# Optimization experiments

Hardware: AMD Instinct MI355X
Metric: run time of the kernel (lower is better)

Reference implementation:

```python
import jax, jax.numpy as jnp
import numpy as np

B, S, E, H = 2, 2048, 2048, 16
HD = E // H  # head dim (value_factor = 1, so key dim == value dim)
EPS = 1e-5


def setup_inputs() -> dict:
    key = jax.random.key(0)
    ks = jax.random.split(key, 12)
    std = 0.02

    def lin(k, din, dout):
        kw, kb = jax.random.split(k)
        W = jax.random.normal(kw, (din, dout), jnp.float32) * std  # stored [in,out]
        b = jnp.zeros((dout,), jnp.float32)
        return W, b

    x = jax.random.normal(ks[0], (B, S, E), jnp.float32)
    Wq, bq = lin(ks[1], E, E)
    Wk, bk = lin(ks[2], E, E)
    Wv, bv = lin(ks[3], E, E)
    Wg, bg = lin(ks[4], E, E)
    Wo, bo = lin(ks[5], E, E)
    gn_w = jnp.ones((E,), jnp.float32)
    gn_b = jnp.zeros((E,), jnp.float32)
    decay = jnp.log(1.0 - 2.0 ** (-5.0 - jnp.arange(H, dtype=jnp.float32)))
    return dict(x=x, Wq=Wq, bq=bq, Wk=Wk, bk=bk, Wv=Wv, bv=bv,
                Wg=Wg, bg=bg, Wo=Wo, bo=bo, gn_w=gn_w, gn_b=gn_b, decay=decay)


def _retention(x, Wq, bq, Wk, bk, Wv, bv, Wg, bg, Wo, bo, gn_w, gn_b, decay):
    b, s, e = x.shape
    h = decay.shape[0]
    hd = e // h
    scaling = hd ** -0.5

    def heads(t):  # [b, s, e] -> [b, h, s, hd]
        return t.reshape(b, s, h, hd).transpose(0, 2, 1, 3)

    q = heads((x @ Wq + bq) * scaling)
    k = heads(x @ Wk + bk)
    v = heads(x @ Wv + bv)

    # causal decay mask D[h,i,j] = gamma_h^(i-j) for i>=j, else 0
    idx = jnp.arange(s)
    diff = idx[:, None] - idx[None, :]               # [s, s]
    causal = diff >= 0
    diff_c = jnp.where(causal, diff, 0).astype(jnp.float32)
    D = jnp.where(causal[None], jnp.exp(decay[:, None, None] * diff_c[None]), 0.0)  # [h,s,s]

    ret = jnp.einsum('bhid,bhjd->bhij', q, k) * D[None]      # [b,h,s,s]
    # per-row abs-sum normalization (detached scale, clamped at 1)
    scale = jnp.clip(jnp.abs(jax.lax.stop_gradient(ret).sum(-1, keepdims=True)), 1.0, None)
    ret = ret / scale
    attn = jnp.einsum('bhij,bhjd->bhid', ret, v)             # [b,h,s,hd]
    attn = attn.transpose(0, 2, 1, 3).reshape(b, s, e)       # [b,s,e]

    # GroupNorm(num_groups=h, num_channels=e) applied per token
    g = attn.reshape(b, s, h, hd)
    mu = g.mean(-1, keepdims=True)
    var = g.var(-1, keepdims=True)
    g = (g - mu) / jnp.sqrt(var + EPS)
    g = g.reshape(b, s, e) * gn_w + gn_b

    gate = jax.nn.silu(x @ Wg + bg)
    return (gate * g) @ Wo + bo


def reference(x, Wq, bq, Wk, bk, Wv, bv, Wg, bg, Wo, bo, gn_w, gn_b, decay):
    return _retention(x, Wq, bq, Wk, bk, Wv, bv, Wg, bg, Wo, bo, gn_w, gn_b, decay)
```

## Files before the change

kernel.cpp:

```cpp
#include <hip/hip_runtime.h>
#include <math.h>

#define Bn 2
#define Sn 2048
#define En 2048
#define Hn 16
#define HDn 128

typedef __attribute__((ext_vector_type(8))) short short8;
typedef __attribute__((ext_vector_type(4))) float f32x4;
typedef unsigned short u16;
typedef unsigned int u32;

__device__ __forceinline__ float bf2f(u16 x){
  union { u32 u; float f; } v; v.u = ((u32)x) << 16; return v.f;
}
__device__ __forceinline__ u16 f2bf(float f){
  union { float f; u32 u; } v; v.f = f;
  u32 r = v.u + 0x7fff + ((v.u >> 16) & 1);
  return (u16)(r >> 16);
}
__device__ __forceinline__ void gload16(const u16* g, u16* l){
  __builtin_amdgcn_global_load_lds((const __attribute__((address_space(1))) void*)g,
                                   (__attribute__((address_space(3))) void*)l, 16, 0, 0);
}

__global__ void detect_dtype(const u16* __restrict__ x, int* __restrict__ flag){
  int lane = threadIdx.x;
  int cnt = 0;
  #pragma unroll
  for (int i = 0; i < 4; i++){
    u16 u = x[lane*4 + i];
    int e = (u >> 7) & 0xFF;
    cnt += (e < 96 || e > 159) ? 1 : 0;
  }
  cnt += __shfl_xor(cnt, 1);  cnt += __shfl_xor(cnt, 2);  cnt += __shfl_xor(cnt, 4);
  cnt += __shfl_xor(cnt, 8);  cnt += __shfl_xor(cnt, 16); cnt += __shfl_xor(cnt, 32);
  if (lane == 0) flag[0] = (cnt > 32) ? 1 : 0;
}

__global__ __launch_bounds__(256) void convert_x(const void* __restrict__ xin, u16* __restrict__ xb,
                                                 const int* __restrict__ flag){
  long i8 = ((long)blockIdx.x*256 + threadIdx.x)*8;
  if (flag[0]){
    const float* xf = (const float*)xin;
    float4 a = *(const float4*)(xf + i8);
    float4 b = *(const float4*)(xf + i8 + 4);
    u16 t[8] = {f2bf(a.x),f2bf(a.y),f2bf(a.z),f2bf(a.w),f2bf(b.x),f2bf(b.y),f2bf(b.z),f2bf(b.w)};
    *(uint4*)(xb + i8) = *(uint4*)t;
  } else {
    *(uint4*)(xb + i8) = *(const uint4*)((const u16*)xin + i8);
  }
}

__global__ __launch_bounds__(256) void transpose2048(const void* __restrict__ in, u16* __restrict__ out,
                                                     const int* __restrict__ flag){
  __shared__ __align__(16) u16 t[64][72];
  int bx = blockIdx.x & 31;
  int by = blockIdx.x >> 5;
  int tid = threadIdx.x;
  int f = flag[0];
  #pragma unroll
  for (int c = tid; c < 512; c += 256){
    int r = c >> 3, col = (c & 7) << 3;
    long base = (long)((by<<6)+r)*2048 + (bx<<6) + col;
    u16 tmp[8];
    if (f){
      const float* pf = (const float*)in + base;
      float4 a = *(const float4*)pf;
      float4 b = *(const float4*)(pf + 4);
      tmp[0]=f2bf(a.x); tmp[1]=f2bf(a.y); tmp[2]=f2bf(a.z); tmp[3]=f2bf(a.w);
      tmp[4]=f2bf(b.x); tmp[5]=f2bf(b.y); tmp[6]=f2bf(b.z); tmp[7]=f2bf(b.w);
    } else {
      *(uint4*)tmp = *(const uint4*)((const u16*)in + base);
    }
    *(uint4*)&t[r][col] = *(uint4*)tmp;
  }
  __syncthreads();
  #pragma unroll
  for (int c = tid; c < 512; c += 256){
    int r = c >> 3, col = (c & 7) << 3;
    u16 tmp[8];
    #pragma unroll
    for (int i = 0; i < 8; i++) tmp[i] = t[col + i][r];
    *(uint4*)(out + (long)((bx<<6)+r)*2048 + (by<<6) + col) = *(uint4*)tmp;
  }
}

__global__ __launch_bounds__(256) void gemm_bt(const u16* __restrict__ A, const u16* __restrict__ Bt,
                const void* __restrict__ bias, void* __restrict__ C,
                int Mdim, int Ndim, int Kdim, int mode, float scale,
                const int* __restrict__ flag, int outfp){
  __shared__ __align__(16) u16 As[128*32];
  __shared__ __align__(16) u16 Bs[128*32];
  int blk = blockIdx.x;
  int st = blk & 7, lid = blk >> 3;
  int m0 = ((st >> 1)*8 + (lid & 7)) << 7;
  int n0 = ((st & 1)*8 + (lid >> 3)) << 7;
  int tid = threadIdx.x;
  int w = tid >> 6, lane = tid & 63, l16 = lane & 15, quad = lane >> 4;
  int wm = w & 1, wn = w >> 1;
  int f = flag[0];
  int sr = lane >> 2;
  int sc = (lane & 3) << 3;
  const u16* gA = A  + (long)(m0 + (w<<5) + sr)*Kdim + sc;
  const u16* gB = Bt + (long)(n0 + (w<<5) + sr)*Kdim + sc;
  u16* lA0 = As + (w<<5)*32;  u16* lA1 = lA0 + 512;
  u16* lB0 = Bs + (w<<5)*32;  u16* lB1 = lB0 + 512;
  const long rowskip = (long)16*Kdim;

  f32x4 acc[4][4];
  #pragma unroll
  for (int i = 0; i < 4; i++)
    #pragma unroll
    for (int j = 0; j < 4; j++) acc[i][j] = (f32x4){0.f,0.f,0.f,0.f};

  for (int k0 = 0; k0 < Kdim; k0 += 32){
    __syncthreads();
    gload16(gA + k0,           lA0);
    gload16(gA + k0 + rowskip, lA1);
    gload16(gB + k0,           lB0);
    gload16(gB + k0 + rowskip, lB1);
    __syncthreads();
    short8 af[4], bfr[4];
    #pragma unroll
    for (int mf = 0; mf < 4; mf++) af[mf]  = *(const short8*)&As[(wm*64 + mf*16 + l16)*32 + quad*8];
    #pragma unroll
    for (int nf = 0; nf < 4; nf++) bfr[nf] = *(const short8*)&Bs[(wn*64 + nf*16 + l16)*32 + quad*8];
    #pragma unroll
    for (int mf = 0; mf < 4; mf++)
      #pragma unroll
      for (int nf = 0; nf < 4; nf++)
        acc[mf][nf] = __builtin_amdgcn_mfma_f32_16x16x32_bf16(af[mf], bfr[nf], acc[mf][nf], 0, 0, 0);
  }
  #pragma unroll
  for (int nf = 0; nf < 4; nf++){
    int col = n0 + wn*64 + nf*16 + l16;
    float bv = f ? ((const float*)bias)[col] : bf2f(((const u16*)bias)[col]);
    #pragma unroll
    for (int mf = 0; mf < 4; mf++){
      #pragma unroll
      for (int r = 0; r < 4; r++){
        int row = m0 + wm*64 + mf*16 + quad*4 + r;
        float v = acc[mf][nf][r] + bv;
        if (mode == 1) v *= scale;
        else if (mode == 2) v = v / (1.0f + __expf(-v));
        long idx = (long)row*Ndim + col;
        if (outfp && f) ((float*)C)[idx] = v;
        else            ((u16*)C)[idx] = f2bf(v);
      }
    }
  }
}

__global__ __launch_bounds__(256) void gemm4(const u16* __restrict__ A, const u16* __restrict__ Wt4,
                const void* __restrict__ bq_, const void* __restrict__ bk_,
                const void* __restrict__ bv_, const void* __restrict__ bg_,
                u16* __restrict__ qo, u16* __restrict__ ko, u16* __restrict__ vo, u16* __restrict__ go,
                const int* __restrict__ flag, float qscale){
  __shared__ __align__(16) u16 As[128*32];
  __shared__ __align__(16) u16 Bs[128*32];
  const int Kdim = 2048, Ndim = 2048;
  const size_t WE = (size_t)2048*2048;
  int blk = blockIdx.x;
  int xcd = blk & 7, lid = blk >> 3;
  int m0 = ((xcd << 2) | (lid & 3)) << 7;
  int n0 = ((lid >> 2) & 15) << 7;
  int wsel = lid >> 6;
  const u16* Bt = Wt4 + WE*(size_t)wsel;
  const void* bias = (wsel==0) ? bq_ : (wsel==1) ? bk_ : (wsel==2) ? bv_ : bg_;
  u16* C = (wsel==0) ? qo : (wsel==1) ? ko : (wsel==2) ? vo : go;
  int tid = threadIdx.x;
  int w = tid >> 6, lane = tid & 63, l16 = lane & 15, quad = lane >> 4;
  int wm = w & 1, wn = w >> 1;
  int f = flag[0];
  int sr = lane >> 2;
  int sc = (lane & 3) << 3;
  const u16* gA = A  + (long)(m0 + (w<<5) + sr)*Kdim + sc;
  const u16* gB = Bt + (long)(n0 + (w<<5) + sr)*Kdim + sc;
  u16* lA0 = As + (w<<5)*32;  u16* lA1 = lA0 + 512;
  u16* lB0 = Bs + (w<<5)*32;  u16* lB1 = lB0 + 512;
  const long rowskip = (long)16*Kdim;

  f32x4 acc[4][4];
  #pragma unroll
  for (int i = 0; i < 4; i++)
    #pragma unroll
    for (int j = 0; j < 4; j++) acc[i][j] = (f32x4){0.f,0.f,0.f,0.f};

  for (int k0 = 0; k0 < Kdim; k0 += 32){
    __syncthreads();
    gload16(gA + k0,           lA0);
    gload16(gA + k0 + rowskip, lA1);
    gload16(gB + k0,           lB0);
    gload16(gB + k0 + rowskip, lB1);
    __syncthreads();
    short8 af[4], bfr[4];
    #pragma unroll
    for (int mf = 0; mf < 4; mf++) af[mf]  = *(const short8*)&As[(wm*64 + mf*16 + l16)*32 + quad*8];
    #pragma unroll
    for (int nf = 0; nf < 4; nf++) bfr[nf] = *(const short8*)&Bs[(wn*64 + nf*16 + l16)*32 + quad*8];
    #pragma unroll
    for (int mf = 0; mf < 4; mf++)
      #pragma unroll
      for (int nf = 0; nf < 4; nf++)
        acc[mf][nf] = __builtin_amdgcn_mfma_f32_16x16x32_bf16(af[mf], bfr[nf], acc[mf][nf], 0, 0, 0);
  }
  #pragma unroll
  for (int nf = 0; nf < 4; nf++){
    int col = n0 + wn*64 + nf*16 + l16;
    float bv = f ? ((const float*)bias)[col] : bf2f(((const u16*)bias)[col]);
    #pragma unroll
    for (int mf = 0; mf < 4; mf++){
      #pragma unroll
      for (int r = 0; r < 4; r++){
        int row = m0 + wm*64 + mf*16 + quad*4 + r;
        float v = acc[mf][nf][r] + bv;
        if (wsel == 0) v *= qscale;
        else if (wsel == 3) v = v / (1.0f + __expf(-v));
        C[(long)row*Ndim + col] = f2bf(v);
      }
    }
  }
}

__global__ __launch_bounds__(256) void retention(const u16* __restrict__ q, const u16* __restrict__ k,
     const u16* __restrict__ v, const u16* __restrict__ gate, const void* __restrict__ gnw,
     const void* __restrict__ gnb, const void* __restrict__ decay, u16* __restrict__ gated,
     const int* __restrict__ flag){
  __shared__ __align__(16) u16 Ks[64][136];
  __shared__ __align__(16) u16 Vt[128][72];
  __shared__ __align__(16) u16 Ss[4][16][72];
  int bh = blockIdx.x & 31;
  int it = 31 - (blockIdx.x >> 5);
  int b = bh >> 4, h = bh & 15;
  int f = flag[0];
  float dec = f ? ((const float*)decay)[h] : bf2f(((const u16*)decay)[h]);
  int tid = threadIdx.x, w = tid >> 6, lane = tid & 63, l16 = lane & 15, quad = lane >> 4;

  float gw8[8], gb8[8];
  #pragma unroll
  for (int nf = 0; nf < 8; nf++){
    int ch = h*HDn + nf*16 + l16;
    gw8[nf] = f ? ((const float*)gnw)[ch] : bf2f(((const u16*)gnw)[ch]);
    gb8[nf] = f ? ((const float*)gnb)[ch] : bf2f(((const u16*)gnb)[ch]);
  }
  float ei4[4], ejl[4];
  #pragma unroll
  for (int r = 0; r < 4; r++) ei4[r] = __expf(dec * (float)(w*16 + quad*4 + r));
  #pragma unroll
  for (int nf = 0; nf < 4; nf++) ejl[nf] = __expf(-dec * (float)(nf*16 + l16));

  int i0 = it << 6;
  short8 qf[4];
  {
    int qrow = i0 + w*16 + l16;
    const u16* qbase = q + (long)(b*Sn + qrow)*En + h*HDn;
    #pragma unroll
    for (int kf = 0; kf < 4; kf++){
      uint4 t = *(const uint4*)(qbase + kf*32 + quad*8);
      qf[kf] = *(short8*)&t;
    }
  }
  f32x4 oacc[8];
  #pragma unroll
  for (int i = 0; i < 8; i++) oacc[i] = (f32x4){0.f,0.f,0.f,0.f};
  float rs[4] = {0.f,0.f,0.f,0.f};

  int njt = it + 1;
  uint4 kreg[4], vreg[4];
  #pragma unroll
  for (int t = 0; t < 4; t++){
    int c = tid + t*256;
    int jr = c >> 4, dc = (c & 15) << 3;
    kreg[t] = *(const uint4*)(k + (long)(b*Sn + jr)*En + h*HDn + dc);
    int jr2 = c & 63, dc2 = (c >> 6) << 3;
    vreg[t] = *(const uint4*)(v + (long)(b*Sn + jr2)*En + h*HDn + dc2);
  }

  for (int jt = 0; jt < njt; jt++){
    int j0 = jt << 6;
    float etile = __expf(dec * (float)(i0 - j0));
    float em[4];
    #pragma unroll
    for (int r = 0; r < 4; r++) em[r] = etile * ei4[r];
    __syncthreads();
    #pragma unroll
    for (int t = 0; t < 4; t++){
      int c = tid + t*256;
      int jr = c >> 4, dc = (c & 15) << 3;
      *(uint4*)&Ks[jr][dc] = kreg[t];
      int jr2 = c & 63, dc2 = (c >> 6) << 3;
      u16 tmp[8]; *(uint4*)tmp = vreg[t];
      #pragma unroll
      for (int i = 0; i < 8; i++) Vt[dc2 + i][jr2] = tmp[i];
    }
    __syncthreads();
    if (jt + 1 < njt){
      int jn = j0 + 64;
      #pragma unroll
      for (int t = 0; t < 4; t++){
        int c = tid + t*256;
        int jr = c >> 4, dc = (c & 15) << 3;
        kreg[t] = *(const uint4*)(k + (long)(b*Sn + jn + jr)*En + h*HDn + dc);
        int jr2 = c & 63, dc2 = (c >> 6) << 3;
        vreg[t] = *(const uint4*)(v + (long)(b*Sn + jn + jr2)*En + h*HDn + dc2);
      }
    }
    #pragma unroll
    for (int nf = 0; nf < 4; nf++){
      f32x4 s = (f32x4){0.f,0.f,0.f,0.f};
      #pragma unroll
      for (int kf = 0; kf < 4; kf++){
        short8 kfr = *(const short8*)&Ks[nf*16 + l16][kf*32 + quad*8];
        s = __builtin_amdgcn_mfma_f32_16x16x32_bf16(qf[kf], kfr, s, 0, 0, 0);
      }
      int j = j0 + nf*16 + l16;
      #pragma unroll
      for (int r = 0; r < 4; r++){
        int i = i0 + w*16 + quad*4 + r;
        float p = s[r] * em[r] * ejl[nf];
        p = (i >= j) ? p : 0.0f;
        rs[r] += p;
        Ss[w][quad*4 + r][nf*16 + l16] = f2bf(p);
      }
    }
    asm volatile("" ::: "memory");
    __builtin_amdgcn_s_waitcnt(0xC07F);
    asm volatile("" ::: "memory");
    #pragma unroll
    for (int kf = 0; kf < 2; kf++){
      short8 pa = *(const short8*)&Ss[w][l16][kf*32 + quad*8];
      #pragma unroll
      for (int nf = 0; nf < 8; nf++){
        short8 vf = *(const short8*)&Vt[nf*16 + l16][kf*32 + quad*8];
        oacc[nf] = __builtin_amdgcn_mfma_f32_16x16x32_bf16(pa, vf, oacc[nf], 0, 0, 0);
      }
    }
  }
  #pragma unroll
  for (int r = 0; r < 4; r++){
    float x = rs[r];
    x += __shfl_xor(x, 1); x += __shfl_xor(x, 2); x += __shfl_xor(x, 4); x += __shfl_xor(x, 8);
    float sc = 1.0f / fmaxf(fabsf(x), 1.0f);
    #pragma unroll
    for (int nf = 0; nf < 8; nf++) oacc[nf][r] *= sc;
  }
  float mu[4], rstd[4];
  #pragma unroll
  for (int r = 0; r < 4; r++){
    float s1 = 0.f, s2 = 0.f;
    #pragma unroll
    for (int nf = 0; nf < 8; nf++){ float xv = oacc[nf][r]; s1 += xv; s2 += xv*xv; }
    s1 += __shfl_xor(s1, 1); s1 += __shfl_xor(s1, 2); s1 += __shfl_xor(s1, 4); s1 += __shfl_xor(s1, 8);
    s2 += __shfl_xor(s2, 1); s2 += __shfl_xor(s2, 2); s2 += __shfl_xor(s2, 4); s2 += __shfl_xor(s2, 8);
    float m = s1 * (1.0f/128.0f);
    float var = s2 * (1.0f/128.0f) - m*m;
    mu[r] = m; rstd[r] = rsqrtf(fmaxf(var, 0.0f) + 1e-5f);
  }
  #pragma unroll
  for (int nf = 0; nf < 8; nf++){
    int ch = h*HDn + nf*16 + l16;
    #pragma unroll
    for (int r = 0; r < 4; r++){
      int row = i0 + w*16 + quad*4 + r;
      long ga = (long)(b*Sn + row)*En + ch;
      float g = (oacc[nf][r] - mu[r]) * rstd[r] * gw8[nf] + gb8[nf];
      float gt = bf2f(gate[ga]);
      gated[ga] = f2bf(gt * g);
    }
  }
}

extern "C" void kernel_launch(void* const* d_in, const int* in_sizes, int n_in,
                              void* d_out, int out_size, void* d_ws, size_t ws_size,
                              hipStream_t stream){
  const void* x   = d_in[0];
  const void* Wq  = d_in[1];
  const void* bq  = d_in[2];
  const void* Wk  = d_in[3];
  const void* bk  = d_in[4];
  const void* Wv  = d_in[5];
  const void* bv  = d_in[6];
  const void* Wg  = d_in[7];
  const void* bg  = d_in[8];
  const void* Wo  = d_in[9];
  const void* bo  = d_in[10];
  const void* gnw = d_in[11];
  const void* gnb = d_in[12];
  const void* dec = d_in[13];

  u16* base = (u16*)d_ws;
  const size_t WE = (size_t)2048*2048;
  const size_t AE = (size_t)4096*2048;
  const float qscale = 0.08838834764831845f;
  u16* gatebuf = (u16*)d_out;

  const size_t fused_bytes = (AE*4 + WE*4)*2 + 64;

  if (ws_size >= fused_bytes){
    u16* xb  = base;
    u16* Wt4 = xb + AE;
    u16* qb  = Wt4 + 4*WE;
    u16* kb  = qb + AE;
    u16* vb  = kb + AE;
    int* flag = (int*)(vb + AE);
    u16* gtd = qb;

    detect_dtype<<<1, 64, 0, stream>>>((const u16*)x, flag);
    convert_x<<<4096, 256, 0, stream>>>(x, xb, flag);
    transpose2048<<<1024, 256, 0, stream>>>(Wq, Wt4,        flag);
    transpose2048<<<1024, 256, 0, stream>>>(Wk, Wt4 + WE,   flag);
    transpose2048<<<1024, 256, 0, stream>>>(Wv, Wt4 + 2*WE, flag);
    transpose2048<<<1024, 256, 0, stream>>>(Wg, Wt4 + 3*WE, flag);

    gemm4<<<2048, 256, 0, stream>>>(xb, Wt4, bq, bk, bv, bg, qb, kb, vb, gatebuf, flag, qscale);

    retention<<<1024, 256, 0, stream>>>(qb, kb, vb, gatebuf, gnw, gnb, dec, gtd, flag);

    transpose2048<<<1024, 256, 0, stream>>>(Wo, Wt4, flag);
    gemm_bt<<<512, 256, 0, stream>>>(gtd, Wt4, bo, d_out, 4096, 2048, 2048, 0, 1.0f, flag, 1);
  } else {
    u16* xb = base;
    u16* Wt = xb + AE;
    u16* qb = Wt + WE;
    u16* kb = qb + AE;
    u16* vb = kb + AE;
    int* flag = (int*)(vb + AE);
    u16* gtd = qb;

    detect_dtype<<<1, 64, 0, stream>>>((const u16*)x, flag);
    convert_x<<<4096, 256, 0, stream>>>(x, xb, flag);

    transpose2048<<<1024, 256, 0, stream>>>(Wq, Wt, flag);
    gemm_bt<<<512, 256, 0, stream>>>(xb, Wt, bq, qb, 4096, 2048, 2048, 1, qscale, flag, 0);
    transpose2048<<<1024, 256, 0, stream>>>(Wk, Wt, flag);
    gemm_bt<<<512, 256, 0, stream>>>(xb, Wt, bk, kb, 4096, 2048, 2048, 0, 1.0f, flag, 0);
    transpose2048<<<1024, 256, 0, stream>>>(Wv, Wt, flag);
    gemm_bt<<<512, 256, 0, stream>>>(xb, Wt, bv, vb, 4096, 2048, 2048, 0, 1.0f, flag, 0);
    transpose2048<<<1024, 256, 0, stream>>>(Wg, Wt, flag);
    gemm_bt<<<512, 256, 0, stream>>>(xb, Wt, bg, gatebuf, 4096, 2048, 2048, 2, 1.0f, flag, 0);

    retention<<<1024, 256, 0, stream>>>(qb, kb, vb, gatebuf, gnw, gnb, dec, gtd, flag);

    transpose2048<<<1024, 256, 0, stream>>>(Wo, Wt, flag);
    gemm_bt<<<512, 256, 0, stream>>>(gtd, Wt, bo, d_out, 4096, 2048, 2048, 0, 1.0f, flag, 1);
  }
}
```

Before: 521.6 us.

## Rewrite QKVG projection GEMM as 256x256 tile, 8-phase double-buffered pipeline

Replaces the 128x128x32 single-buffered fused QKV+gate GEMM with a 256x256 tile, K-step 64 kernel using 512 threads and double-buffered LDS. LDS uses an XOR swizzle. Global-to-LDS loads are interleaved across eight MFMA phases with explicit waitcnt, barriers and setprio. The goal is to hide global load latency, cut synchronisation and bank conflicts, and raise MFMA utilisation. In exchange it uses 128KB of LDS and many accumulator registers, and the hand-tuned waitcnt counts leave little margin for errors.

```diff
diff --git a/kernel.cpp b/kernel.cpp
--- a/kernel.cpp
+++ b/kernel.cpp
@@ -153,72 +153,156 @@
   }
 }
 
-__global__ __launch_bounds__(256) void gemm4(const u16* __restrict__ A, const u16* __restrict__ Wt4,
+__global__ __launch_bounds__(512, 2) void gemm4_8ph(const u16* __restrict__ A, const u16* __restrict__ Wt4,
                 const void* __restrict__ bq_, const void* __restrict__ bk_,
                 const void* __restrict__ bv_, const void* __restrict__ bg_,
                 u16* __restrict__ qo, u16* __restrict__ ko, u16* __restrict__ vo, u16* __restrict__ go,
                 const int* __restrict__ flag, float qscale){
-  __shared__ __align__(16) u16 As[128*32];
-  __shared__ __align__(16) u16 Bs[128*32];
-  const int Kdim = 2048, Ndim = 2048;
+  __shared__ __align__(16) u16 As[2][16384];
+  __shared__ __align__(16) u16 Bs[2][16384];
   const size_t WE = (size_t)2048*2048;
   int blk = blockIdx.x;
   int xcd = blk & 7, lid = blk >> 3;
-  int m0 = ((xcd << 2) | (lid & 3)) << 7;
-  int n0 = ((lid >> 2) & 15) << 7;
-  int wsel = lid >> 6;
+  int m0 = (((xcd << 1) | (lid & 1))) << 8;
+  int n0 = ((lid >> 1) & 7) << 8;
+  int wsel = (lid >> 4) & 3;
   const u16* Bt = Wt4 + WE*(size_t)wsel;
   const void* bias = (wsel==0) ? bq_ : (wsel==1) ? bk_ : (wsel==2) ? bv_ : bg_;
-  u16* C = (wsel==0) ? qo : (wsel==1) ? ko : (wsel==2) ? vo : go;
+  u16* Cout = (wsel==0) ? qo : (wsel==1) ? ko : (wsel==2) ? vo : go;
   int tid = threadIdx.x;
   int w = tid >> 6, lane = tid & 63, l16 = lane & 15, quad = lane >> 4;
-  int wm = w & 1, wn = w >> 1;
+  int wm = w >> 2, wn = w & 3;
   int f = flag[0];
-  int sr = lane >> 2;
-  int sc = (lane & 3) << 3;
-  const u16* gA = A  + (long)(m0 + (w<<5) + sr)*Kdim + sc;
-  const u16* gB = Bt + (long)(n0 + (w<<5) + sr)*Kdim + sc;
-  u16* lA0 = As + (w<<5)*32;  u16* lA1 = lA0 + 512;
-  u16* lB0 = Bs + (w<<5)*32;  u16* lB1 = lB0 + 512;
-  const long rowskip = (long)16*Kdim;
-
-  f32x4 acc[4][4];
-  #pragma unroll
-  for (int i = 0; i < 4; i++)
+
+  int srowA = tid >> 3;
+  int srowB = ((w >> 2) << 6) | ((w & 3) << 3) | ((tid >> 3) & 7);
+  int sg = ((tid & 7) ^ ((tid >> 3) & 7)) << 3;
+  const u16* gA = A  + (long)(m0 + srowA)*2048 + sg;
+  const u16* gB = Bt + (long)(n0 + srowB)*2048 + sg;
+  u16* ldsA = &As[0][0];
+  u16* ldsB = &Bs[0][0];
+  const int wofsA = w << 9;
+  const int wofsB = ((w >> 2) << 12) | ((w & 3) << 9);
+
+  int g0 = quad ^ (l16 & 7);
+  const int abase = (wm*128 + l16) * 64;
+  const int bbase = (wn*64  + l16) * 64;
+
+  f32x4 acc[8][4];
+  #pragma unroll
+  for (int i = 0; i < 8; i++)
     #pragma unroll
     for (int j = 0; j < 4; j++) acc[i][j] = (f32x4){0.f,0.f,0.f,0.f};
-
-  for (int k0 = 0; k0 < Kdim; k0 += 32){
-    __syncthreads();
-    gload16(gA + k0,           lA0);
-    gload16(gA + k0 + rowskip, lA1);
-    gload16(gB + k0,           lB0);
-    gload16(gB + k0 + rowskip, lB1);
-    __syncthreads();
-    short8 af[4], bfr[4];
-    #pragma unroll
-    for (int mf = 0; mf < 4; mf++) af[mf]  = *(const short8*)&As[(wm*64 + mf*16 + l16)*32 + quad*8];
-    #pragma unroll
-    for (int nf = 0; nf < 4; nf++) bfr[nf] = *(const short8*)&Bs[(wn*64 + nf*16 + l16)*32 + quad*8];
-    #pragma unroll
-    for (int mf = 0; mf < 4; mf++)
-      #pragma unroll
-      for (int nf = 0; nf < 4; nf++)
-        acc[mf][nf] = __builtin_amdgcn_mfma_f32_16x16x32_bf16(af[mf], bfr[nf], acc[mf][nf], 0, 0, 0);
-  }
+  short8 a[4][2], b[2][2];
+
+#define STG_A(buf, tt, h) do{ \
+  gload16(gA + (long)((h)*64)*2048       + (tt)*64, ldsA + (buf)*16384 + (h)*4096 + wofsA); \
+  gload16(gA + (long)(128 + (h)*64)*2048 + (tt)*64, ldsA + (buf)*16384 + 8192 + (h)*4096 + wofsA); \
+}while(0)
+#define STG_B(buf, tt, h) do{ \
+  gload16(gB + (long)((h)*32)*2048       + (tt)*64, ldsB + (buf)*16384 + (h)*2048 + wofsB); \
+  gload16(gB + (long)(128 + (h)*32)*2048 + (tt)*64, ldsB + (buf)*16384 + 8192 + (h)*2048 + wofsB); \
+}while(0)
+#define LDA_Q(buf, qm) do{ \
+  _Pragma("unroll") for (int m_ = 0; m_ < 4; m_++) \
+  _Pragma("unroll") for (int ks_ = 0; ks_ < 2; ks_++) \
+    a[m_][ks_] = *(const short8*)(ldsA + (buf)*16384 + abase + ((qm)*64 + m_*16)*64 + ((g0 ^ (ks_<<2))<<3)); \
+}while(0)
+#define LDB_Q(buf, qn) do{ \
+  _Pragma("unroll") for (int n_ = 0; n_ < 2; n_++) \
+  _Pragma("unroll") for (int ks_ = 0; ks_ < 2; ks_++) \
+    b[n_][ks_] = *(const short8*)(ldsB + (buf)*16384 + bbase + (((qn)*2 + n_)*16)*64 + ((g0 ^ (ks_<<2))<<3)); \
+}while(0)
+#define MFMAQ(qm, qn) do{ \
+  _Pragma("unroll") for (int ks_ = 0; ks_ < 2; ks_++) \
+  _Pragma("unroll") for (int m_ = 0; m_ < 4; m_++) \
+  _Pragma("unroll") for (int n_ = 0; n_ < 2; n_++) \
+    acc[(qm)*4 + m_][(qn)*2 + n_] = __builtin_amdgcn_mfma_f32_16x16x32_bf16( \
+        a[m_][ks_], b[n_][ks_], acc[(qm)*4 + m_][(qn)*2 + n_], 0, 0, 0); \
+}while(0)
+#define PH_TAIL(qm, qn) do{ \
+  asm volatile("" ::: "memory"); \
+  __builtin_amdgcn_s_barrier(); \
+  asm volatile("s_waitcnt lgkmcnt(0)" ::: "memory"); \
+  __builtin_amdgcn_sched_barrier(0); \
+  __builtin_amdgcn_s_setprio(1); \
+  MFMAQ(qm, qn); \
+  __builtin_amdgcn_s_setprio(0); \
+  __builtin_amdgcn_sched_barrier(0); \
+  asm volatile("" ::: "memory"); \
+  __builtin_amdgcn_s_barrier(); \
+}while(0)
+
+  STG_A(0, 0, 0);
+  STG_B(0, 0, 1);
+  STG_A(0, 0, 1);
+  STG_B(0, 0, 0);
+  STG_A(1, 1, 0);
+  STG_B(1, 1, 1);
+  STG_A(1, 1, 1);
+  asm volatile("s_waitcnt vmcnt(6)" ::: "memory");
+  __builtin_amdgcn_s_barrier();
+
+  #pragma unroll 1
+  for (int i = 0; i < 16; i++){
+    const int t = i << 1;
+    const bool full = (i < 15);
+    LDA_Q(0, 0); LDB_Q(0, 0);
+    STG_B(1, t + 1, 0);
+    asm volatile("s_waitcnt lgkmcnt(8)" ::: "memory");
+    PH_TAIL(0, 0);
+    LDB_Q(0, 1);
+    if (full) STG_A(0, t + 2, 0);
+    PH_TAIL(0, 1);
+    LDA_Q(0, 1);
+    if (full) STG_B(0, t + 2, 1);
+    PH_TAIL(1, 1);
+    LDB_Q(0, 0);
+    if (full){
+      STG_A(0, t + 2, 1);
+      asm volatile("s_waitcnt vmcnt(6)" ::: "memory");
+    } else {
+      asm volatile("s_waitcnt vmcnt(0)" ::: "memory");
+    }
+    PH_TAIL(1, 0);
+    LDA_Q(1, 0); LDB_Q(1, 0);
+    if (full) STG_B(0, t + 2, 0);
+    asm volatile("s_waitcnt lgkmcnt(8)" ::: "memory");
+    PH_TAIL(0, 0);
+    LDB_Q(1, 1);
+    if (full) STG_A(1, t + 3, 0);
+    PH_TAIL(0, 1);
+    LDA_Q(1, 1);
+    if (full) STG_B(1, t + 3, 1);
+    PH_TAIL(1, 1);
+    LDB_Q(1, 0);
+    if (full){
+      STG_A(1, t + 3, 1);
+      asm volatile("s_waitcnt vmcnt(6)" ::: "memory");
+    }
+    PH_TAIL(1, 0);
+  }
+
+#undef STG_A
+#undef STG_B
+#undef LDA_Q
+#undef LDB_Q
+#undef MFMAQ
+#undef PH_TAIL
+
   #pragma unroll
   for (int nf = 0; nf < 4; nf++){
     int col = n0 + wn*64 + nf*16 + l16;
     float bv = f ? ((const float*)bias)[col] : bf2f(((const u16*)bias)[col]);
     #pragma unroll
-    for (int mf = 0; mf < 4; mf++){
+    for (int mf = 0; mf < 8; mf++){
       #pragma unroll
       for (int r = 0; r < 4; r++){
-        int row = m0 + wm*64 + mf*16 + quad*4 + r;
+        int row = m0 + wm*128 + mf*16 + quad*4 + r;
         float v = acc[mf][nf][r] + bv;
         if (wsel == 0) v *= qscale;
         else if (wsel == 3) v = v / (1.0f + __expf(-v));
-        C[(long)row*Ndim + col] = f2bf(v);
+        Cout[(long)row*2048 + col] = f2bf(v);
       }
     }
   }
@@ -414,7 +498,7 @@
     transpose2048<<<1024, 256, 0, stream>>>(Wv, Wt4 + 2*WE, flag);
     transpose2048<<<1024, 256, 0, stream>>>(Wg, Wt4 + 3*WE, flag);
 
-    gemm4<<<2048, 256, 0, stream>>>(xb, Wt4, bq, bk, bv, bg, qb, kb, vb, gatebuf, flag, qscale);
+    gemm4_8ph<<<512, 512, 0, stream>>>(xb, Wt4, bq, bk, bv, bg, qb, kb, vb, gatebuf, flag, qscale);
 
     retention<<<1024, 256, 0, stream>>>(qb, kb, vb, gatebuf, gnw, gnb, dec, gtd, flag);
 
```

Result: no change. 512.3 us (-1.8%).
